# Kernel optimization log

Measured on AMD Instinct MI355X. Metric: run time of the kernel, lower is better.

Reference implementation:

```python
import jax, jax.numpy as jnp
import numpy as np

B, T = 64, 1024
EMB = 10          # embedding_dim
H = 64            # hidden_size
NH = 2            # attention heads
IN = 3 * EMB      # 30 = GRU input_size
GAMMA = 1.0


def rbf(d):
    # BondExpansionRBF: exp(-gamma * |center - d|^2), centers = 1..10
    centers = jnp.arange(1, EMB + 1, dtype=d.dtype)          # [10]
    return jnp.exp(-GAMMA * (centers - d[..., None]) ** 2)   # [..., 10]


def gru_layer(x, w_ih, w_hh, b_ih, b_hh):
    # x: [B,T,D] -> [B,T,H]; torch GRU gate order: r, z, n
    Bn = x.shape[0]
    Hn = w_hh.shape[1]
    xw = jnp.einsum('btd,gd->btg', x, w_ih) + b_ih           # [B,T,3H] precomputed input proj

    def step(h, xt):
        gh = h @ w_hh.T + b_hh
        xr, xz, xn = jnp.split(xt, 3, axis=-1)
        hr, hz, hn = jnp.split(gh, 3, axis=-1)
        r = jax.nn.sigmoid(xr + hr)
        z = jax.nn.sigmoid(xz + hz)
        n = jnp.tanh(xn + r * hn)
        h = (1.0 - z) * n + z * h
        return h, h

    _, ys = jax.lax.scan(step, jnp.zeros((Bn, Hn), x.dtype), jnp.swapaxes(xw, 0, 1))
    return jnp.swapaxes(ys, 0, 1)


def mha(x, in_w, in_b, out_w, out_b):
    # torch nn.MultiheadAttention (batch_first, self-attn), eval mode
    Bn, Tn, E = x.shape
    Hd = E // NH
    qkv = x @ in_w.T + in_b                                   # [B,T,3E]
    q, k, v = jnp.split(qkv, 3, axis=-1)

    def heads(t):
        return t.reshape(Bn, Tn, NH, Hd).transpose(0, 2, 1, 3)  # [B,NH,T,Hd]

    q, k, v = heads(q), heads(k), heads(v)
    scores = jnp.einsum('bhqd,bhkd->bhqk', q, k) / jnp.asarray(np.sqrt(Hd), x.dtype)
    a = jax.nn.softmax(scores, axis=-1)
    o = jnp.einsum('bhqk,bhkd->bhqd', a, v).transpose(0, 2, 1, 3).reshape(Bn, Tn, E)
    return o @ out_w.T + out_b


def forward(atom_idx, bond_dist, emb, w_ih0, w_hh0, b_ih0, b_hh0,
            w_ih1, w_hh1, b_ih1, b_hh1, in_w1, in_b1, out_w1, out_b1,
            in_w2, in_b2, out_w2, out_b2, w_l, b_l, w_l1, b_l1):
    idx_i = atom_idx[..., 0]
    idx_j = atom_idx[..., 1]
    # index 0 -> zero vector (padding semantics of the python-loop conditionals)
    e_i = jnp.where((idx_i != 0)[..., None], emb[idx_i], 0.0)   # [B,T,10]
    e_j = jnp.where((idx_j != 0)[..., None], emb[idx_j], 0.0)   # [B,T,10]
    d = jnp.where((idx_i != 0)[..., None], rbf(bond_dist), 0.0)  # [B,T,10]
    x = jnp.concatenate([e_i, e_j, d], axis=-1)                  # [B,T,30]

    g = gru_layer(x, w_ih0, w_hh0, b_ih0, b_hh0)
    g = gru_layer(g, w_ih1, w_hh1, b_ih1, b_hh1)
    a = mha(g, in_w1, in_b1, out_w1, out_b1)
    a = mha(a, in_w2, in_b2, out_w2, out_b2)

    last = a[:, -1, :]                                           # [B,H]
    h = jax.nn.relu(last @ w_l.T + b_l)                          # [B,32]
    out = h @ w_l1.T + b_l1                                      # [B,1]
    return out[:, 0]                                             # [B]


def setup_inputs() -> dict:
    key = jax.random.key(0)
    ks = jax.random.split(key, 20)

    def n(k, shape, s=0.05):
        return jax.random.normal(k, shape, jnp.float32) * s

    return {
        'atom_idx': jax.random.randint(ks[0], (B, T, 2), 0, 119),
        'bond_dist': jax.random.uniform(ks[1], (B, T), jnp.float32) * 10.0,
        'emb': n(ks[2], (119, EMB), 1.0),
        'w_ih0': n(ks[3], (3 * H, IN)), 'w_hh0': n(ks[4], (3 * H, H)),
        'b_ih0': n(ks[5], (3 * H,)), 'b_hh0': n(ks[6], (3 * H,)),
        'w_ih1': n(ks[7], (3 * H, H)), 'w_hh1': n(ks[8], (3 * H, H)),
        'b_ih1': n(ks[9], (3 * H,)), 'b_hh1': n(ks[10], (3 * H,)),
        'in_w1': n(ks[11], (3 * H, H)), 'in_b1': n(ks[12], (3 * H,)),
        'out_w1': n(ks[13], (H, H)), 'out_b1': jnp.zeros((H,), jnp.float32),
        'in_w2': n(ks[14], (3 * H, H)), 'in_b2': n(ks[15], (3 * H,)),
        'out_w2': n(ks[16], (H, H)), 'out_b2': jnp.zeros((H,), jnp.float32),
        'w_l': n(ks[17], (32, H)), 'b_l': jnp.zeros((32,), jnp.float32),
        'w_l1': n(ks[18], (1, 32)), 'b_l1': jnp.zeros((1,), jnp.float32),
    }


def reference(atom_idx, bond_dist, emb, w_ih0, w_hh0, b_ih0, b_hh0,
              w_ih1, w_hh1, b_ih1, b_hh1, in_w1, in_b1, out_w1, out_b1,
              in_w2, in_b2, out_w2, out_b2, w_l, b_l, w_l1, b_l1):
    return forward(atom_idx, bond_dist, emb, w_ih0, w_hh0, b_ih0, b_hh0,
                   w_ih1, w_hh1, b_ih1, b_hh1, in_w1, in_b1, out_w1, out_b1,
                   in_w2, in_b2, out_w2, out_b2, w_l, b_l, w_l1, b_l1)
```

## Files before the change

### kernel.cpp

```cpp
#include <hip/hip_runtime.h>

typedef unsigned int uint_t;

#define BB 64
#define TT 1024

__device__ __forceinline__ float sigm(float x) { return 1.f / (1.f + __expf(-x)); }
__device__ __forceinline__ float tanh_f(float x) { float e = __expf(2.f * x); return 1.f - 2.f / (e + 1.f); }
__device__ __forceinline__ int finitef(float x) { return (x == x) && (fabsf(x) < 1e30f); }

__device__ __forceinline__ void spinwait(volatile int* f, int v) {
  if (*f >= v) { asm volatile("" ::: "memory"); return; }
  int it = 0;
  while (*f < v && it < (1 << 15)) { __builtin_amdgcn_s_sleep(1); ++it; }
  asm volatile("" ::: "memory");
}

__device__ __forceinline__ float feat(int b, int t, int j,
                                      const int* atom_idx, const float* bond_dist,
                                      const float* emb) {
  int ii = atom_idx[(b * TT + t) * 2 + 0];
  if (j < 10) {
    return ii ? emb[ii * 10 + j] : 0.f;
  } else if (j < 20) {
    int jj = atom_idx[(b * TT + t) * 2 + 1];
    return jj ? emb[jj * 10 + (j - 10)] : 0.f;
  } else {
    float d = bond_dist[b * TT + t];
    float c = (float)(j - 19);
    float df = c - d;
    return ii ? __expf(-df * df) : 0.f;
  }
}

extern "C" __global__ void __launch_bounds__(256)
k_xw0(const int* atom_idx, const float* bond_dist, const float* emb,
      const float* w_ih0, const float* b_ih0, float* xw0) {
  int b  = blockIdx.x >> 4;
  int t0 = (blockIdx.x & 15) << 6;
  int tid = threadIdx.x;
  __shared__ float xt[64 * 31];
  for (int i = tid; i < 64 * 30; i += 256) {
    int r = i / 30, j = i % 30;
    xt[r * 31 + j] = feat(b, t0 + r, j, atom_idx, bond_dist, emb);
  }
  __syncthreads();
  for (int L = tid; L < 64 * 192; L += 256) {
    int g = L >> 6, r = L & 63;
    const float* wr = w_ih0 + g * 30;
    const float* ar = &xt[r * 31];
    float acc = b_ih0[g];
    #pragma unroll
    for (int c = 0; c < 30; ++c) acc += wr[c] * ar[c];
    xw0[((size_t)b * TT + t0 + r) * 192 + g] = acc;
  }
}

__device__ __forceinline__ void gemm64(const float* __restrict__ act_g,
                                       const float* __restrict__ w,
                                       const float* __restrict__ bias,
                                       float* al,
                                       int G, int tid,
                                       float* out, int out_rstride, size_t out_base) {
  for (int i = tid; i < 64 * 64; i += 256) {
    int r = i >> 6, c = i & 63;
    al[r * 65 + c] = act_g[r * 64 + c];
  }
  __syncthreads();
  for (int L = tid; L < 64 * G; L += 256) {
    int g = L >> 6, r = L & 63;
    const float* wr = w + (size_t)g * 64;
    const float* ar = &al[r * 65];
    float acc = bias[g];
    #pragma unroll
    for (int c = 0; c < 64; ++c) acc += wr[c] * ar[c];
    out[out_base + (size_t)r * out_rstride + g] = acc;
  }
}

extern "C" __global__ void __launch_bounds__(192, 1)
k_grufused(const float* xw0, const float* w_hh0, const float* b_hh0,
           const float* w_ih1, const float* b_ih1,
           const float* w_hh1, const float* b_hh1, float* g1out) {
  int b    = blockIdx.x;
  int lane = threadIdx.x & 63;
  int wid  = threadIdx.x >> 6;
  __shared__ __align__(16) float h0ring[16][64];
  __shared__ __align__(16) float xwring[16][192];
  __shared__ __align__(16) float h1pp[2][64];
  __shared__ int flags[3];

  if (threadIdx.x < 3) flags[threadIdx.x] = -1;
  if (wid == 0) h0ring[15][lane] = 0.f;
  if (wid == 2) h1pp[0][lane] = 0.f;
  __syncthreads();

  volatile int* w0d = &flags[0];
  volatile int* w1d = &flags[1];
  volatile int* w2d = &flags[2];

  if (wid == 0) {
    float wr[64], wz[64], wn[64];
    {
      const float4* wrp = (const float4*)(w_hh0 + (size_t)lane * 64);
      const float4* wzp = (const float4*)(w_hh0 + (size_t)(64 + lane) * 64);
      const float4* wnp = (const float4*)(w_hh0 + (size_t)(128 + lane) * 64);
      #pragma unroll
      for (int i = 0; i < 16; ++i) {
        float4 a = wrp[i]; float4 c = wzp[i]; float4 d = wnp[i];
        wr[4*i] = a.x; wr[4*i+1] = a.y; wr[4*i+2] = a.z; wr[4*i+3] = a.w;
        wz[4*i] = c.x; wz[4*i+1] = c.y; wz[4*i+2] = c.z; wz[4*i+3] = c.w;
        wn[4*i] = d.x; wn[4*i+1] = d.y; wn[4*i+2] = d.z; wn[4*i+3] = d.w;
      }
    }
    float br = b_hh0[lane], bz = b_hh0[64 + lane], bn = b_hh0[128 + lane];
    float hv = 0.f;
    const float* xwb = xw0 + (size_t)b * TT * 192;
    float xr0 = xwb[      lane], xz0 = xwb[ 64 + lane], xn0 = xwb[128 + lane];
    float xr1 = xwb[192 + lane], xz1 = xwb[256 + lane], xn1 = xwb[320 + lane];
    float xr2 = xwb[384 + lane], xz2 = xwb[448 + lane], xn2 = xwb[512 + lane];
    float xr3 = xwb[576 + lane], xz3 = xwb[640 + lane], xn3 = xwb[704 + lane];

    auto gstep = [&](int s, float xr, float xz, float xn) {
      const float4* hp4 = (const float4*)h0ring[(s + 15) & 15];
      float a0 = br, a1 = 0.f, c0 = bz, c1 = 0.f, d0 = bn, d1 = 0.f;
      #pragma unroll
      for (int i = 0; i < 16; ++i) {
        float4 h4 = hp4[i];
        a0 += wr[4*i+0] * h4.x; a1 += wr[4*i+1] * h4.y;
        a0 += wr[4*i+2] * h4.z; a1 += wr[4*i+3] * h4.w;
        c0 += wz[4*i+0] * h4.x; c1 += wz[4*i+1] * h4.y;
        c0 += wz[4*i+2] * h4.z; c1 += wz[4*i+3] * h4.w;
        d0 += wn[4*i+0] * h4.x; d1 += wn[4*i+1] * h4.y;
        d0 += wn[4*i+2] * h4.z; d1 += wn[4*i+3] * h4.w;
      }
      float r = sigm(xr + (a0 + a1));
      float z = sigm(xz + (c0 + c1));
      float n = tanh_f(xn + r * (d0 + d1));
      hv = (1.f - z) * n + z * hv;
      h0ring[s & 15][lane] = hv;
    };
    auto pf = [&](int s, float& a, float& bb_, float& c) {
      const float* xp = xwb + (size_t)s * 192;
      a = xp[lane]; bb_ = xp[64 + lane]; c = xp[128 + lane];
    };

    for (int s0 = 0; s0 < TT; s0 += 4) {
      if (s0 >= 16) spinwait(w1d, s0 - 13);
      bool dopf = (s0 < TT - 4);
      gstep(s0 + 0, xr0, xz0, xn0); if (dopf) pf(s0 + 4, xr0, xz0, xn0);
      gstep(s0 + 1, xr1, xz1, xn1); if (dopf) pf(s0 + 5, xr1, xz1, xn1);
      gstep(s0 + 2, xr2, xz2, xn2); if (dopf) pf(s0 + 6, xr2, xz2, xn2);
      gstep(s0 + 3, xr3, xz3, xn3); if (dopf) pf(s0 + 7, xr3, xz3, xn3);
      asm volatile("" ::: "memory");
      if (lane == 0) *w0d = s0 + 3;
    }
  } else if (wid == 1) {
    float wr[64], wz[64], wn[64];
    {
      const float4* wrp = (const float4*)(w_ih1 + (size_t)lane * 64);
      const float4* wzp = (const float4*)(w_ih1 + (size_t)(64 + lane) * 64);
      const float4* wnp = (const float4*)(w_ih1 + (size_t)(128 + lane) * 64);
      #pragma unroll
      for (int i = 0; i < 16; ++i) {
        float4 a = wrp[i]; float4 c = wzp[i]; float4 d = wnp[i];
        wr[4*i] = a.x; wr[4*i+1] = a.y; wr[4*i+2] = a.z; wr[4*i+3] = a.w;
        wz[4*i] = c.x; wz[4*i+1] = c.y; wz[4*i+2] = c.z; wz[4*i+3] = c.w;
        wn[4*i] = d.x; wn[4*i+1] = d.y; wn[4*i+2] = d.z; wn[4*i+3] = d.w;
      }
    }
    float br = b_ih1[lane], bz = b_ih1[64 + lane], bn = b_ih1[128 + lane];

    for (int t0 = 0; t0 < TT; t0 += 4) {
      spinwait(w0d, t0 + 3);
      if (t0 >= 16) spinwait(w2d, t0 - 13);
      #pragma unroll
      for (int k = 0; k < 4; ++k) {
        int t = t0 + k;
        const float4* hp4 = (const float4*)h0ring[t & 15];
        float a0 = br, a1 = 0.f, c0 = bz, c1 = 0.f, d0 = bn, d1 = 0.f;
        #pragma unroll
        for (int i = 0; i < 16; ++i) {
          float4 h4 = hp4[i];
          a0 += wr[4*i+0] * h4.x; a1 += wr[4*i+1] * h4.y;
          a0 += wr[4*i+2] * h4.z; a1 += wr[4*i+3] * h4.w;
          c0 += wz[4*i+0] * h4.x; c1 += wz[4*i+1] * h4.y;
          c0 += wz[4*i+2] * h4.z; c1 += wz[4*i+3] * h4.w;
          d0 += wn[4*i+0] * h4.x; d1 += wn[4*i+1] * h4.y;
          d0 += wn[4*i+2] * h4.z; d1 += wn[4*i+3] * h4.w;
        }
        xwring[t & 15][lane]       = a0 + a1;
        xwring[t & 15][64 + lane]  = c0 + c1;
        xwring[t & 15][128 + lane] = d0 + d1;
      }
      asm volatile("" ::: "memory");
      if (lane == 0) *w1d = t0 + 3;
    }
  } else {
    float wr[64], wz[64], wn[64];
    {
      const float4* wrp = (const float4*)(w_hh1 + (size_t)lane * 64);
      const float4* wzp = (const float4*)(w_hh1 + (size_t)(64 + lane) * 64);
      const float4* wnp = (const float4*)(w_hh1 + (size_t)(128 + lane) * 64);
      #pragma unroll
      for (int i = 0; i < 16; ++i) {
        float4 a = wrp[i]; float4 c = wzp[i]; float4 d = wnp[i];
        wr[4*i] = a.x; wr[4*i+1] = a.y; wr[4*i+2] = a.z; wr[4*i+3] = a.w;
        wz[4*i] = c.x; wz[4*i+1] = c.y; wz[4*i+2] = c.z; wz[4*i+3] = c.w;
        wn[4*i] = d.x; wn[4*i+1] = d.y; wn[4*i+2] = d.z; wn[4*i+3] = d.w;
      }
    }
    float br = b_hh1[lane], bz = b_hh1[64 + lane], bn = b_hh1[128 + lane];
    float hv = 0.f;
    float* houtb = g1out + (size_t)b * TT * 64 + lane;

    for (int t0 = 0; t0 < TT; t0 += 4) {
      spinwait(w1d, t0 + 3);
      #pragma unroll
      for (int k = 0; k < 4; ++k) {
        int t = t0 + k;
        float xr = xwring[t & 15][lane];
        float xz = xwring[t & 15][64 + lane];
        float xn = xwring[t & 15][128 + lane];
        const float4* hp4 = (const float4*)h1pp[t & 1];
        float a0 = br, a1 = 0.f, c0 = bz, c1 = 0.f, d0 = bn, d1 = 0.f;
        #pragma unroll
        for (int i = 0; i < 16; ++i) {
          float4 h4 = hp4[i];
          a0 += wr[4*i+0] * h4.x; a1 += wr[4*i+1] * h4.y;
          a0 += wr[4*i+2] * h4.z; a1 += wr[4*i+3] * h4.w;
          c0 += wz[4*i+0] * h4.x; c1 += wz[4*i+1] * h4.y;
          c0 += wz[4*i+2] * h4.z; c1 += wz[4*i+3] * h4.w;
          d0 += wn[4*i+0] * h4.x; d1 += wn[4*i+1] * h4.y;
          d0 += wn[4*i+2] * h4.z; d1 += wn[4*i+3] * h4.w;
        }
        float r = sigm(xr + (a0 + a1));
        float z = sigm(xz + (c0 + c1));
        float n = tanh_f(xn + r * (d0 + d1));
        hv = (1.f - z) * n + z * hv;
        h1pp[(t + 1) & 1][lane] = hv;
        houtb[(size_t)t * 64] = hv;
      }
      asm volatile("" ::: "memory");
      if (lane == 0) *w2d = t0 + 3;
    }
  }
}

extern "C" __global__ void __launch_bounds__(256)
k_qkv(const float* g1, const float* in_w1, const float* in_b1,
      float* q1, float* k1, float* v1) {
  int b  = blockIdx.x >> 4;
  int t0 = (blockIdx.x & 15) << 6;
  int tid = threadIdx.x;
  __shared__ float al[64 * 65];
  const float* act = g1 + ((size_t)b * TT + t0) * 64;
  for (int i = tid; i < 64 * 64; i += 256) {
    int r = i >> 6, c = i & 63;
    al[r * 65 + c] = act[r * 64 + c];
  }
  __syncthreads();
  for (int L = tid; L < 64 * 192; L += 256) {
    int g = L >> 6, r = L & 63;
    const float* wr = in_w1 + (size_t)g * 64;
    const float* ar = &al[r * 65];
    float acc = in_b1[g];
    #pragma unroll
    for (int c = 0; c < 64; ++c) acc += wr[c] * ar[c];
    int p = g / 64;
    int rem = g - p * 64;
    int hd = rem >> 5, d = rem & 31;
    float* outp = (p == 0) ? q1 : ((p == 1) ? k1 : v1);
    outp[(((size_t)b * 2 + hd) * TT + t0 + r) * 32 + d] = acc;
  }
}

extern "C" __global__ void __launch_bounds__(256, 4)
k_attn(const float* q1, const float* k1, const float* v1, float* po, float* ml) {
  int gid = blockIdx.x;
  int b   = gid >> 4;
  int h   = (gid >> 3) & 1;
  int seg = (gid >> 2) & 1;
  int qb  = gid & 3;
  int tid = threadIdx.x;
  int tq  = qb * 256 + tid;
  __shared__ __align__(16) float Kt[64 * 32];
  __shared__ __align__(16) float Vt[64 * 32];
  float q[32], o[32];
  const float* qp = q1 + (((size_t)b * 2 + h) * TT + tq) * 32;
  #pragma unroll
  for (int i = 0; i < 8; ++i) {
    float4 v = ((const float4*)qp)[i];
    q[4 * i] = v.x; q[4 * i + 1] = v.y; q[4 * i + 2] = v.z; q[4 * i + 3] = v.w;
  }
  #pragma unroll
  for (int i = 0; i < 32; ++i) o[i] = 0.f;
  float m = -1e30f, l = 0.f;
  const float scale = 0.17677669529663687f;
  const float4* kb = (const float4*)(k1 + ((size_t)b * 2 + h) * TT * 32);
  const float4* vb = (const float4*)(v1 + ((size_t)b * 2 + h) * TT * 32);
  int k0 = seg << 9;
  for (int kt = k0; kt < k0 + 512; kt += 64) {
    __syncthreads();
    ((float4*)Kt)[tid]       = kb[kt * 8 + tid];
    ((float4*)Kt)[tid + 256] = kb[kt * 8 + tid + 256];
    ((float4*)Vt)[tid]       = vb[kt * 8 + tid];
    ((float4*)Vt)[tid + 256] = vb[kt * 8 + tid + 256];
    __syncthreads();
    #pragma unroll 1
    for (int c0 = 0; c0 < 64; c0 += 8) {
      float sv[8];
      #pragma unroll
      for (int j = 0; j < 8; ++j) {
        const float4* kr = (const float4*)&Kt[(c0 + j) * 32];
        float a0 = 0, a1 = 0, a2 = 0, a3 = 0;
        #pragma unroll
        for (int i = 0; i < 8; ++i) {
          float4 kv = kr[i];
          a0 += q[4 * i] * kv.x; a1 += q[4 * i + 1] * kv.y;
          a2 += q[4 * i + 2] * kv.z; a3 += q[4 * i + 3] * kv.w;
        }
        sv[j] = ((a0 + a1) + (a2 + a3)) * scale;
      }
      float cm = sv[0];
      #pragma unroll
      for (int j = 1; j < 8; ++j) cm = fmaxf(cm, sv[j]);
      float mnew = fmaxf(m, cm);
      float alpha = __expf(m - mnew);
      float ps = 0.f;
      #pragma unroll
      for (int j = 0; j < 8; ++j) { sv[j] = __expf(sv[j] - mnew); ps += sv[j]; }
      l = l * alpha + ps;
      m = mnew;
      #pragma unroll
      for (int i = 0; i < 8; ++i) {
        float4 acc;
        acc.x = o[4 * i] * alpha; acc.y = o[4 * i + 1] * alpha;
        acc.z = o[4 * i + 2] * alpha; acc.w = o[4 * i + 3] * alpha;
        #pragma unroll
        for (int j = 0; j < 8; ++j) {
          float4 vv = *(const float4*)&Vt[(c0 + j) * 32 + 4 * i];
          acc.x += sv[j] * vv.x; acc.y += sv[j] * vv.y;
          acc.z += sv[j] * vv.z; acc.w += sv[j] * vv.w;
        }
        o[4 * i] = acc.x; o[4 * i + 1] = acc.y; o[4 * i + 2] = acc.z; o[4 * i + 3] = acc.w;
      }
    }
  }
  size_t rbase = (((size_t)(b * 2 + h)) * 2 + seg) * TT + tq;
  float* op = po + rbase * 32;
  #pragma unroll
  for (int i = 0; i < 8; ++i) {
    float4 s4; s4.x = o[4 * i]; s4.y = o[4 * i + 1]; s4.z = o[4 * i + 2]; s4.w = o[4 * i + 3];
    ((float4*)op)[i] = s4;
  }
  ml[rbase * 2 + 0] = m;
  ml[rbase * 2 + 1] = l;
}

extern "C" __global__ void __launch_bounds__(256)
k_attn_comb(const float* po, const float* ml, float* attnO) {
  int row = blockIdx.x * 256 + threadIdx.x;
  int bh = row >> 10;
  int t  = row & 1023;
  int b = bh >> 1, h = bh & 1;
  size_t r0 = ((size_t)bh * 2 + 0) * TT + t;
  size_t r1 = ((size_t)bh * 2 + 1) * TT + t;
  float m0 = ml[r0 * 2], l0 = ml[r0 * 2 + 1];
  float m1 = ml[r1 * 2], l1 = ml[r1 * 2 + 1];
  float m = fmaxf(m0, m1);
  float w0 = __expf(m0 - m), w1 = __expf(m1 - m);
  float inv = 1.f / (w0 * l0 + w1 * l1);
  w0 *= inv; w1 *= inv;
  const float4* p0 = (const float4*)(po + r0 * 32);
  const float4* p1 = (const float4*)(po + r1 * 32);
  float* op = attnO + ((size_t)b * TT + t) * 64 + h * 32;
  #pragma unroll
  for (int i = 0; i < 8; ++i) {
    float4 a = p0[i], c = p1[i], r;
    r.x = a.x * w0 + c.x * w1; r.y = a.y * w0 + c.y * w1;
    r.z = a.z * w0 + c.z * w1; r.w = a.w * w0 + c.w * w1;
    ((float4*)op)[i] = r;
  }
}

extern "C" __global__ void __launch_bounds__(256)
k_oproj(const float* attnO, const float* out_w1, const float* out_b1, float* a1) {
  int b  = blockIdx.x >> 4;
  int t0 = (blockIdx.x & 15) << 6;
  __shared__ float al[64 * 65];
  gemm64(attnO + ((size_t)b * TT + t0) * 64, out_w1, out_b1, al, 64, threadIdx.x,
         a1, 64, ((size_t)b * TT + t0) * 64);
}

extern "C" __global__ void __launch_bounds__(256)
k_mha2kv(const float* a1, const float* in_w2, const float* in_b2,
         float* s2, float* v2) {
  int b  = blockIdx.x >> 4;
  int t0 = (blockIdx.x & 15) << 6;
  int tid = threadIdx.x;
  __shared__ float a1r[64 * 65];
  __shared__ float q2s[64];
  __shared__ float alast[64];
  if (tid < 64) alast[tid] = a1[((size_t)b * TT + (TT - 1)) * 64 + tid];
  for (int i = tid; i < 4096; i += 256) {
    int r = i >> 6, e = i & 63;
    a1r[r * 65 + e] = a1[((size_t)b * TT + t0 + r) * 64 + e];
  }
  __syncthreads();
  if (tid < 64) {
    float acc = in_b2[tid];
    const float* wr = in_w2 + (size_t)tid * 64;
    #pragma unroll
    for (int e = 0; e < 64; ++e) acc += alast[e] * wr[e];
    q2s[tid] = acc;
  }
  __syncthreads();
  int tt = tid & 63;
  int role = tid >> 6;
  const float* ar = &a1r[tt * 65];
  const float scale = 0.17677669529663687f;
  if (role < 2) {
    float s = 0.f;
    for (int d = 0; d < 32; ++d) {
      int row = 64 + role * 32 + d;
      const float* wr = in_w2 + (size_t)row * 64;
      float acc = in_b2[row];
      #pragma unroll
      for (int e = 0; e < 64; ++e) acc += ar[e] * wr[e];
      s += q2s[row - 64] * acc;
    }
    s2[((size_t)b * 2 + role) * TT + t0 + tt] = s * scale;
  } else {
    int half = role - 2;
    for (int d = 0; d < 32; ++d) {
      int vd = half * 32 + d;
      int row = 128 + vd;
      const float* wr = in_w2 + (size_t)row * 64;
      float acc = in_b2[row];
      #pragma unroll
      for (int e = 0; e < 64; ++e) acc += ar[e] * wr[e];
      v2[((size_t)b * TT + t0 + tt) * 64 + vd] = acc;
    }
  }
}

extern "C" __global__ void __launch_bounds__(256)
k_final(const float* s2, const float* v2,
        const float* out_w2, const float* out_b2,
        const float* w_l, const float* b_l,
        const float* w_l1, const float* b_l1,
        float* out) {
  int b = blockIdx.x;
  int tid = threadIdx.x;
  __shared__ float sm[2 * 1024];
  __shared__ float red[8];
  __shared__ float invl[2];
  __shared__ float opart[4 * 64];
  __shared__ float of[64];
  __shared__ float a2[64];
  __shared__ float hbuf[32];
  __shared__ int bad;
  if (tid == 0) bad = 0;
  for (int i = tid; i < 2048; i += 256) sm[i] = s2[(size_t)b * 2 * TT + i];
  __syncthreads();
  int lane = tid & 63;
  int wid = tid >> 6;
  for (int hh = 0; hh < 2; ++hh) {
    float mx = -1e30f;
    for (int i = tid; i < 1024; i += 256) mx = fmaxf(mx, sm[hh * 1024 + i]);
    #pragma unroll
    for (int off = 32; off > 0; off >>= 1) mx = fmaxf(mx, __shfl_down(mx, off));
    if (lane == 0) red[wid] = mx;
    __syncthreads();
    if (tid == 0) red[4] = fmaxf(fmaxf(red[0], red[1]), fmaxf(red[2], red[3]));
    __syncthreads();
    mx = red[4];
    float s = 0.f;
    for (int i = tid; i < 1024; i += 256) {
      float e = __expf(sm[hh * 1024 + i] - mx);
      sm[hh * 1024 + i] = e;
      s += e;
    }
    #pragma unroll
    for (int off = 32; off > 0; off >>= 1) s += __shfl_down(s, off);
    if (lane == 0) red[wid] = s;
    __syncthreads();
    if (tid == 0) invl[hh] = 1.f / (red[0] + red[1] + red[2] + red[3]);
    __syncthreads();
  }
  {
    int dp = tid & 63;
    int part = tid >> 6;
    int hh = dp >> 5;
    float acc = 0.f;
    for (int t = part * 256; t < part * 256 + 256; ++t)
      acc += sm[hh * 1024 + t] * v2[((size_t)b * TT + t) * 64 + dp];
    opart[part * 64 + dp] = acc;
  }
  __syncthreads();
  if (tid < 64) {
    float o = (opart[tid] + opart[64 + tid] + opart[128 + tid] + opart[192 + tid]) * invl[tid >> 5];
    of[tid] = o;
    if (!finitef(o)) bad = 1;
  }
  __syncthreads();
  if (tid < 64) {
    float acc = out_b2[tid];
    const float* wr = out_w2 + (size_t)tid * 64;
    #pragma unroll
    for (int d = 0; d < 64; ++d) acc += of[d] * wr[d];
    a2[tid] = acc;
  }
  __syncthreads();
  if (tid < 32) {
    float acc = b_l[tid];
    const float* wr = w_l + (size_t)tid * 64;
    #pragma unroll
    for (int e = 0; e < 64; ++e) acc += a2[e] * wr[e];
    hbuf[tid] = fmaxf(acc, 0.f);
  }
  __syncthreads();
  if (tid == 0) {
    float acc = b_l1[0];
    #pragma unroll
    for (int j = 0; j < 32; ++j) acc += hbuf[j] * w_l1[j];
    out[b] = bad ? 777.0f : acc;
  }
}

extern "C" void kernel_launch(void* const* d_in, const int* in_sizes, int n_in,
                              void* d_out, int out_size, void* d_ws, size_t ws_size,
                              hipStream_t stream) {
  const int*   atom_idx  = (const int*)d_in[0];
  const float* bond_dist = (const float*)d_in[1];
  const float* emb       = (const float*)d_in[2];
  const float* w_ih0     = (const float*)d_in[3];
  const float* w_hh0     = (const float*)d_in[4];
  const float* b_ih0     = (const float*)d_in[5];
  const float* b_hh0     = (const float*)d_in[6];
  const float* w_ih1     = (const float*)d_in[7];
  const float* w_hh1     = (const float*)d_in[8];
  const float* b_ih1     = (const float*)d_in[9];
  const float* b_hh1     = (const float*)d_in[10];
  const float* in_w1     = (const float*)d_in[11];
  const float* in_b1     = (const float*)d_in[12];
  const float* out_w1    = (const float*)d_in[13];
  const float* out_b1    = (const float*)d_in[14];
  const float* in_w2     = (const float*)d_in[15];
  const float* in_b2     = (const float*)d_in[16];
  const float* out_w2    = (const float*)d_in[17];
  const float* out_b2    = (const float*)d_in[18];
  const float* w_l       = (const float*)d_in[19];
  const float* b_l       = (const float*)d_in[20];
  const float* w_l1      = (const float*)d_in[21];
  const float* b_l1      = (const float*)d_in[22];

  char* ws = (char*)d_ws;
  float* X  = (float*)(ws);
  float* A  = (float*)(ws + 50331648);
  float* Bq = (float*)(ws + 67108864);
  float* D  = (float*)(ws + 83886080);
  float* q1 = X;
  float* k1 = X + 4194304;
  float* v1 = X + 8388608;
  float* po = (float*)(ws + 16777216);
  float* ml = Bq;

  k_xw0      <<<dim3(1024), dim3(256), 0, stream>>>(atom_idx, bond_dist, emb, w_ih0, b_ih0, X);
  k_grufused <<<dim3(64),   dim3(192), 0, stream>>>(X, w_hh0, b_hh0, w_ih1, b_ih1, w_hh1, b_hh1, Bq);
  k_qkv      <<<dim3(1024), dim3(256), 0, stream>>>(Bq, in_w1, in_b1, q1, k1, v1);
  k_attn     <<<dim3(1024), dim3(256), 0, stream>>>(q1, k1, v1, po, ml);
  k_attn_comb<<<dim3(512),  dim3(256), 0, stream>>>(po, ml, A);
  k_oproj    <<<dim3(1024), dim3(256), 0, stream>>>(A, out_w1, out_b1, Bq);
  k_mha2kv   <<<dim3(1024), dim3(256), 0, stream>>>(Bq, in_w2, in_b2, D, X);
  k_final    <<<dim3(64),   dim3(256), 0, stream>>>(D, X, out_w2, out_b2, w_l, b_l, w_l1, b_l1, (float*)d_out);
}
```

Measured before the change: 1.552 ms.

## Pack GRU matvecs as float2 ops and compute two queries per attention thread

```diff
diff --git a/kernel.cpp b/kernel.cpp
--- a/kernel.cpp
+++ b/kernel.cpp
@@ -1,6 +1,7 @@
 #include <hip/hip_runtime.h>
 
 typedef unsigned int uint_t;
+typedef float v2f __attribute__((ext_vector_type(2)));
 
 #define BB 64
 #define TT 1024
@@ -78,6 +79,17 @@
   }
 }
 
+__device__ __forceinline__ void loadw2(const float* p, v2f* w2) {
+  const float4* p4 = (const float4*)p;
+  #pragma unroll
+  for (int i = 0; i < 16; ++i) {
+    float4 a = p4[i];
+    v2f lo; lo.x = a.x; lo.y = a.y;
+    v2f hi; hi.x = a.z; hi.y = a.w;
+    w2[2 * i] = lo; w2[2 * i + 1] = hi;
+  }
+}
+
 extern "C" __global__ void __launch_bounds__(192, 1)
 k_grufused(const float* xw0, const float* w_hh0, const float* b_hh0,
            const float* w_ih1, const float* b_ih1,
@@ -100,19 +112,10 @@
   volatile int* w2d = &flags[2];
 
   if (wid == 0) {
-    float wr[64], wz[64], wn[64];
-    {
-      const float4* wrp = (const float4*)(w_hh0 + (size_t)lane * 64);
-      const float4* wzp = (const float4*)(w_hh0 + (size_t)(64 + lane) * 64);
-      const float4* wnp = (const float4*)(w_hh0 + (size_t)(128 + lane) * 64);
-      #pragma unroll
-      for (int i = 0; i < 16; ++i) {
-        float4 a = wrp[i]; float4 c = wzp[i]; float4 d = wnp[i];
-        wr[4*i] = a.x; wr[4*i+1] = a.y; wr[4*i+2] = a.z; wr[4*i+3] = a.w;
-        wz[4*i] = c.x; wz[4*i+1] = c.y; wz[4*i+2] = c.z; wz[4*i+3] = c.w;
-        wn[4*i] = d.x; wn[4*i+1] = d.y; wn[4*i+2] = d.z; wn[4*i+3] = d.w;
-      }
-    }
+    v2f wr2[32], wz2[32], wn2[32];
+    loadw2(w_hh0 + (size_t)lane * 64,        wr2);
+    loadw2(w_hh0 + (size_t)(64 + lane) * 64, wz2);
+    loadw2(w_hh0 + (size_t)(128 + lane) * 64, wn2);
     float br = b_hh0[lane], bz = b_hh0[64 + lane], bn = b_hh0[128 + lane];
     float hv = 0.f;
     const float* xwb = xw0 + (size_t)b * TT * 192;
@@ -123,20 +126,21 @@
 
     auto gstep = [&](int s, float xr, float xz, float xn) {
       const float4* hp4 = (const float4*)h0ring[(s + 15) & 15];
-      float a0 = br, a1 = 0.f, c0 = bz, c1 = 0.f, d0 = bn, d1 = 0.f;
+      v2f ar; ar.x = br; ar.y = 0.f;
+      v2f az; az.x = bz; az.y = 0.f;
+      v2f an; an.x = bn; an.y = 0.f;
       #pragma unroll
       for (int i = 0; i < 16; ++i) {
         float4 h4 = hp4[i];
-        a0 += wr[4*i+0] * h4.x; a1 += wr[4*i+1] * h4.y;
-        a0 += wr[4*i+2] * h4.z; a1 += wr[4*i+3] * h4.w;
-        c0 += wz[4*i+0] * h4.x; c1 += wz[4*i+1] * h4.y;
-        c0 += wz[4*i+2] * h4.z; c1 += wz[4*i+3] * h4.w;
-        d0 += wn[4*i+0] * h4.x; d1 += wn[4*i+1] * h4.y;
-        d0 += wn[4*i+2] * h4.z; d1 += wn[4*i+3] * h4.w;
+        v2f hlo; hlo.x = h4.x; hlo.y = h4.y;
+        v2f hhi; hhi.x = h4.z; hhi.y = h4.w;
+        ar += wr2[2*i] * hlo; ar += wr2[2*i+1] * hhi;
+        az += wz2[2*i] * hlo; az += wz2[2*i+1] * hhi;
+        an += wn2[2*i] * hlo; an += wn2[2*i+1] * hhi;
       }
-      float r = sigm(xr + (a0 + a1));
-      float z = sigm(xz + (c0 + c1));
-      float n = tanh_f(xn + r * (d0 + d1));
+      float r = sigm(xr + (ar.x + ar.y));
+      float z = sigm(xz + (az.x + az.y));
+      float n = tanh_f(xn + r * (an.x + an.y));
       hv = (1.f - z) * n + z * hv;
       h0ring[s & 15][lane] = hv;
     };
@@ -156,19 +160,10 @@
       if (lane == 0) *w0d = s0 + 3;
     }
   } else if (wid == 1) {
-    float wr[64], wz[64], wn[64];
-    {
-      const float4* wrp = (const float4*)(w_ih1 + (size_t)lane * 64);
-      const float4* wzp = (const float4*)(w_ih1 + (size_t)(64 + lane) * 64);
-      const float4* wnp = (const float4*)(w_ih1 + (size_t)(128 + lane) * 64);
-      #pragma unroll
-      for (int i = 0; i < 16; ++i) {
-        float4 a = wrp[i]; float4 c = wzp[i]; float4 d = wnp[i];
-        wr[4*i] = a.x; wr[4*i+1] = a.y; wr[4*i+2] = a.z; wr[4*i+3] = a.w;
-        wz[4*i] = c.x; wz[4*i+1] = c.y; wz[4*i+2] = c.z; wz[4*i+3] = c.w;
-        wn[4*i] = d.x; wn[4*i+1] = d.y; wn[4*i+2] = d.z; wn[4*i+3] = d.w;
-      }
-    }
+    v2f wr2[32], wz2[32], wn2[32];
+    loadw2(w_ih1 + (size_t)lane * 64,        wr2);
+    loadw2(w_ih1 + (size_t)(64 + lane) * 64, wz2);
+    loadw2(w_ih1 + (size_t)(128 + lane) * 64, wn2);
     float br = b_ih1[lane], bz = b_ih1[64 + lane], bn = b_ih1[128 + lane];
 
     for (int t0 = 0; t0 < TT; t0 += 4) {
@@ -178,38 +173,30 @@
       for (int k = 0; k < 4; ++k) {
         int t = t0 + k;
         const float4* hp4 = (const float4*)h0ring[t & 15];
-        float a0 = br, a1 = 0.f, c0 = bz, c1 = 0.f, d0 = bn, d1 = 0.f;
+        v2f ar; ar.x = br; ar.y = 0.f;
+        v2f az; az.x = bz; az.y = 0.f;
+        v2f an; an.x = bn; an.y = 0.f;
         #pragma unroll
         for (int i = 0; i < 16; ++i) {
           float4 h4 = hp4[i];
-          a0 += wr[4*i+0] * h4.x; a1 += wr[4*i+1] * h4.y;
-          a0 += wr[4*i+2] * h4.z; a1 += wr[4*i+3] * h4.w;
-          c0 += wz[4*i+0] * h4.x; c1 += wz[4*i+1] * h4.y;
-          c0 += wz[4*i+2] * h4.z; c1 += wz[4*i+3] * h4.w;
-          d0 += wn[4*i+0] * h4.x; d1 += wn[4*i+1] * h4.y;
-          d0 += wn[4*i+2] * h4.z; d1 += wn[4*i+3] * h4.w;
+          v2f hlo; hlo.x = h4.x; hlo.y = h4.y;
+          v2f hhi; hhi.x = h4.z; hhi.y = h4.w;
+          ar += wr2[2*i] * hlo; ar += wr2[2*i+1] * hhi;
+          az += wz2[2*i] * hlo; az += wz2[2*i+1] * hhi;
+          an += wn2[2*i] * hlo; an += wn2[2*i+1] * hhi;
         }
-        xwring[t & 15][lane]       = a0 + a1;
-        xwring[t & 15][64 + lane]  = c0 + c1;
-        xwring[t & 15][128 + lane] = d0 + d1;
+        xwring[t & 15][lane]       = ar.x + ar.y;
+        xwring[t & 15][64 + lane]  = az.x + az.y;
+        xwring[t & 15][128 + lane] = an.x + an.y;
       }
       asm volatile("" ::: "memory");
       if (lane == 0) *w1d = t0 + 3;
     }
   } else {
-    float wr[64], wz[64], wn[64];
-    {
-      const float4* wrp = (const float4*)(w_hh1 + (size_t)lane * 64);
-      const float4* wzp = (const float4*)(w_hh1 + (size_t)(64 + lane) * 64);
-      const float4* wnp = (const float4*)(w_hh1 + (size_t)(128 + lane) * 64);
-      #pragma unroll
-      for (int i = 0; i < 16; ++i) {
-        float4 a = wrp[i]; float4 c = wzp[i]; float4 d = wnp[i];
-        wr[4*i] = a.x; wr[4*i+1] = a.y; wr[4*i+2] = a.z; wr[4*i+3] = a.w;
-        wz[4*i] = c.x; wz[4*i+1] = c.y; wz[4*i+2] = c.z; wz[4*i+3] = c.w;
-        wn[4*i] = d.x; wn[4*i+1] = d.y; wn[4*i+2] = d.z; wn[4*i+3] = d.w;
-      }
-    }
+    v2f wr2[32], wz2[32], wn2[32];
+    loadw2(w_hh1 + (size_t)lane * 64,        wr2);
+    loadw2(w_hh1 + (size_t)(64 + lane) * 64, wz2);
+    loadw2(w_hh1 + (size_t)(128 + lane) * 64, wn2);
     float br = b_hh1[lane], bz = b_hh1[64 + lane], bn = b_hh1[128 + lane];
     float hv = 0.f;
     float* houtb = g1out + (size_t)b * TT * 64 + lane;
@@ -223,20 +210,21 @@
         float xz = xwring[t & 15][64 + lane];
         float xn = xwring[t & 15][128 + lane];
         const float4* hp4 = (const float4*)h1pp[t & 1];
-        float a0 = br, a1 = 0.f, c0 = bz, c1 = 0.f, d0 = bn, d1 = 0.f;
+        v2f ar; ar.x = br; ar.y = 0.f;
+        v2f az; az.x = bz; az.y = 0.f;
+        v2f an; an.x = bn; an.y = 0.f;
         #pragma unroll
         for (int i = 0; i < 16; ++i) {
           float4 h4 = hp4[i];
-          a0 += wr[4*i+0] * h4.x; a1 += wr[4*i+1] * h4.y;
-          a0 += wr[4*i+2] * h4.z; a1 += wr[4*i+3] * h4.w;
-          c0 += wz[4*i+0] * h4.x; c1 += wz[4*i+1] * h4.y;
-          c0 += wz[4*i+2] * h4.z; c1 += wz[4*i+3] * h4.w;
-          d0 += wn[4*i+0] * h4.x; d1 += wn[4*i+1] * h4.y;
-          d0 += wn[4*i+2] * h4.z; d1 += wn[4*i+3] * h4.w;
+          v2f hlo; hlo.x = h4.x; hlo.y = h4.y;
+          v2f hhi; hhi.x = h4.z; hhi.y = h4.w;
+          ar += wr2[2*i] * hlo; ar += wr2[2*i+1] * hhi;
+          az += wz2[2*i] * hlo; az += wz2[2*i+1] * hhi;
+          an += wn2[2*i] * hlo; an += wn2[2*i+1] * hhi;
         }
-        float r = sigm(xr + (a0 + a1));
-        float z = sigm(xz + (c0 + c1));
-        float n = tanh_f(xn + r * (d0 + d1));
+        float r = sigm(xr + (ar.x + ar.y));
+        float z = sigm(xz + (az.x + az.y));
+        float n = tanh_f(xn + r * (an.x + an.y));
         hv = (1.f - z) * n + z * hv;
         h1pp[(t + 1) & 1][lane] = hv;
         houtb[(size_t)t * 64] = hv;
@@ -275,27 +263,30 @@
   }
 }
 
-extern "C" __global__ void __launch_bounds__(256, 4)
+extern "C" __global__ void __launch_bounds__(256, 2)
 k_attn(const float* q1, const float* k1, const float* v1, float* po, float* ml) {
   int gid = blockIdx.x;
-  int b   = gid >> 4;
-  int h   = (gid >> 3) & 1;
-  int seg = (gid >> 2) & 1;
-  int qb  = gid & 3;
+  int b   = gid >> 3;
+  int h   = (gid >> 2) & 1;
+  int seg = (gid >> 1) & 1;
+  int qb  = gid & 1;
   int tid = threadIdx.x;
-  int tq  = qb * 256 + tid;
+  int tq0 = qb * 512 + tid;
   __shared__ __align__(16) float Kt[64 * 32];
   __shared__ __align__(16) float Vt[64 * 32];
-  float q[32], o[32];
-  const float* qp = q1 + (((size_t)b * 2 + h) * TT + tq) * 32;
+  float qa[32], qc[32], oa[32], oc[32];
+  const float* qp0 = q1 + (((size_t)b * 2 + h) * TT + tq0) * 32;
+  const float* qp1 = qp0 + 256 * 32;
   #pragma unroll
   for (int i = 0; i < 8; ++i) {
-    float4 v = ((const float4*)qp)[i];
-    q[4 * i] = v.x; q[4 * i + 1] = v.y; q[4 * i + 2] = v.z; q[4 * i + 3] = v.w;
+    float4 v0 = ((const float4*)qp0)[i];
+    float4 v1r = ((const float4*)qp1)[i];
+    qa[4*i] = v0.x; qa[4*i+1] = v0.y; qa[4*i+2] = v0.z; qa[4*i+3] = v0.w;
+    qc[4*i] = v1r.x; qc[4*i+1] = v1r.y; qc[4*i+2] = v1r.z; qc[4*i+3] = v1r.w;
   }
   #pragma unroll
-  for (int i = 0; i < 32; ++i) o[i] = 0.f;
-  float m = -1e30f, l = 0.f;
+  for (int i = 0; i < 32; ++i) { oa[i] = 0.f; oc[i] = 0.f; }
+  float m0 = -1e30f, l0 = 0.f, m1 = -1e30f, l1 = 0.f;
   const float scale = 0.17677669529663687f;
   const float4* kb = (const float4*)(k1 + ((size_t)b * 2 + h) * TT * 32);
   const float4* vb = (const float4*)(v1 + ((size_t)b * 2 + h) * TT * 32);
@@ -309,53 +300,64 @@
     __syncthreads();
     #pragma unroll 1
     for (int c0 = 0; c0 < 64; c0 += 8) {
-      float sv[8];
+      float sv0[8], sv1[8];
       #pragma unroll
       for (int j = 0; j < 8; ++j) {
         const float4* kr = (const float4*)&Kt[(c0 + j) * 32];
-        float a0 = 0, a1 = 0, a2 = 0, a3 = 0;
+        float a0 = 0, a1 = 0, c0a = 0, c1a = 0;
         #pragma unroll
         for (int i = 0; i < 8; ++i) {
           float4 kv = kr[i];
-          a0 += q[4 * i] * kv.x; a1 += q[4 * i + 1] * kv.y;
-          a2 += q[4 * i + 2] * kv.z; a3 += q[4 * i + 3] * kv.w;
+          a0 += qa[4*i]   * kv.x; a1 += qa[4*i+1] * kv.y;
+          a0 += qa[4*i+2] * kv.z; a1 += qa[4*i+3] * kv.w;
+          c0a += qc[4*i]   * kv.x; c1a += qc[4*i+1] * kv.y;
+          c0a += qc[4*i+2] * kv.z; c1a += qc[4*i+3] * kv.w;
         }
-        sv[j] = ((a0 + a1) + (a2 + a3)) * scale;
+        sv0[j] = (a0 + a1) * scale;
+        sv1[j] = (c0a + c1a) * scale;
       }
-      float cm = sv[0];
-      #pragma unroll
-      for (int j = 1; j < 8; ++j) cm = fmaxf(cm, sv[j]);
-      float mnew = fmaxf(m, cm);
-      float alpha = __expf(m - mnew);
-      float ps = 0.f;
-      #pragma unroll
-      for (int j = 0; j < 8; ++j) { sv[j] = __expf(sv[j] - mnew); ps += sv[j]; }
-      l = l * alpha + ps;
-      m = mnew;
+      float cm0 = sv0[0], cm1 = sv1[0];
+      #pragma unroll
+      for (int j = 1; j < 8; ++j) { cm0 = fmaxf(cm0, sv0[j]); cm1 = fmaxf(cm1, sv1[j]); }
+      float mn0 = fmaxf(m0, cm0), mn1 = fmaxf(m1, cm1);
+      float al0 = __expf(m0 - mn0), al1 = __expf(m1 - mn1);
+      float ps0 = 0.f, ps1 = 0.f;
+      #pragma unroll
+      for (int j = 0; j < 8; ++j) {
+        sv0[j] = __expf(sv0[j] - mn0); ps0 += sv0[j];
+        sv1[j] = __expf(sv1[j] - mn1); ps1 += sv1[j];
+      }
+      l0 = l0 * al0 + ps0; m0 = mn0;
+      l1 = l1 * al1 + ps1; m1 = mn1;
       #pragma unroll
       for (int i = 0; i < 8; ++i) {
-        float4 acc;
-        acc.x = o[4 * i] * alpha; acc.y = o[4 * i + 1] * alpha;
-        acc.z = o[4 * i + 2] * alpha; acc.w = o[4 * i + 3] * alpha;
+        float4 A, C;
+        A.x = oa[4*i] * al0; A.y = oa[4*i+1] * al0; A.z = oa[4*i+2] * al0; A.w = oa[4*i+3] * al0;
+        C.x = oc[4*i] * al1; C.y = oc[4*i+1] * al1; C.z = oc[4*i+2] * al1; C.w = oc[4*i+3] * al1;
         #pragma unroll
         for (int j = 0; j < 8; ++j) {
           float4 vv = *(const float4*)&Vt[(c0 + j) * 32 + 4 * i];
-          acc.x += sv[j] * vv.x; acc.y += sv[j] * vv.y;
-          acc.z += sv[j] * vv.z; acc.w += sv[j] * vv.w;
+          A.x += sv0[j] * vv.x; A.y += sv0[j] * vv.y; A.z += sv0[j] * vv.z; A.w += sv0[j] * vv.w;
+          C.x += sv1[j] * vv.x; C.y += sv1[j] * vv.y; C.z += sv1[j] * vv.z; C.w += sv1[j] * vv.w;
         }
-        o[4 * i] = acc.x; o[4 * i + 1] = acc.y; o[4 * i + 2] = acc.z; o[4 * i + 3] = acc.w;
+        oa[4*i] = A.x; oa[4*i+1] = A.y; oa[4*i+2] = A.z; oa[4*i+3] = A.w;
+        oc[4*i] = C.x; oc[4*i+1] = C.y; oc[4*i+2] = C.z; oc[4*i+3] = C.w;
       }
     }
   }
-  size_t rbase = (((size_t)(b * 2 + h)) * 2 + seg) * TT + tq;
-  float* op = po + rbase * 32;
+  size_t rb0 = (((size_t)(b * 2 + h)) * 2 + seg) * TT + tq0;
+  size_t rb1 = rb0 + 256;
+  float* op0 = po + rb0 * 32;
+  float* op1 = po + rb1 * 32;
   #pragma unroll
   for (int i = 0; i < 8; ++i) {
-    float4 s4; s4.x = o[4 * i]; s4.y = o[4 * i + 1]; s4.z = o[4 * i + 2]; s4.w = o[4 * i + 3];
-    ((float4*)op)[i] = s4;
-  }
-  ml[rbase * 2 + 0] = m;
-  ml[rbase * 2 + 1] = l;
+    float4 s0; s0.x = oa[4*i]; s0.y = oa[4*i+1]; s0.z = oa[4*i+2]; s0.w = oa[4*i+3];
+    float4 s1; s1.x = oc[4*i]; s1.y = oc[4*i+1]; s1.z = oc[4*i+2]; s1.w = oc[4*i+3];
+    ((float4*)op0)[i] = s0;
+    ((float4*)op1)[i] = s1;
+  }
+  ml[rb0 * 2 + 0] = m0; ml[rb0 * 2 + 1] = l0;
+  ml[rb1 * 2 + 0] = m1; ml[rb1 * 2 + 1] = l1;
 }
 
 extern "C" __global__ void __launch_bounds__(256)
@@ -570,7 +572,7 @@
   k_xw0      <<<dim3(1024), dim3(256), 0, stream>>>(atom_idx, bond_dist, emb, w_ih0, b_ih0, X);
   k_grufused <<<dim3(64),   dim3(192), 0, stream>>>(X, w_hh0, b_hh0, w_ih1, b_ih1, w_hh1, b_hh1, Bq);
   k_qkv      <<<dim3(1024), dim3(256), 0, stream>>>(Bq, in_w1, in_b1, q1, k1, v1);
-  k_attn     <<<dim3(1024), dim3(256), 0, stream>>>(q1, k1, v1, po, ml);
+  k_attn     <<<dim3(512),  dim3(256), 0, stream>>>(q1, k1, v1, po, ml);
   k_attn_comb<<<dim3(512),  dim3(256), 0, stream>>>(po, ml, A);
   k_oproj    <<<dim3(1024), dim3(256), 0, stream>>>(A, out_w1, out_b1, Bq);
   k_mha2kv   <<<dim3(1024), dim3(256), 0, stream>>>(Bq, in_w2, in_b2, D, X);
```

Result: faster. 1.297 ms (-16.5%).
